# Kernel tuning notes

Hardware: AMD Instinct MI355X
Metric: run time of the kernel (lower is better)

Reference implementation:

```python
import jax, jax.numpy as jnp
import numpy as np


def setup_inputs() -> dict:
    key = jax.random.key(0)
    k1, k2, k3, k4, k5 = jax.random.split(key, 5)
    B, S, IN, OUT, R = 4, 2048, 4096, 4096, 16
    x = jax.random.normal(k1, (B, S, IN), dtype=jnp.float32)
    weight = jax.random.normal(k2, (OUT, IN), dtype=jnp.float32) * 0.02
    bias = jax.random.normal(k3, (OUT,), dtype=jnp.float32) * 0.02
    lora_A = jax.random.normal(k4, (R, IN), dtype=jnp.float32) * 0.02
    lora_B = jax.random.normal(k5, (OUT, R), dtype=jnp.float32) * 0.02
    return {"x": x, "weight": weight, "bias": bias, "lora_A": lora_A, "lora_B": lora_B}


def reference(x, weight, bias, lora_A, lora_B):
    # HiRA (Linear path): out = x @ (W * (1 + A^T B^T)^T)^T + bias
    # prod_AB[i, o] = sum_r A[r, i] * B[o, r]; adapted_weight[o, i] = W[o, i] * (prod_AB + 1)[i, o]
    prod_AB = jnp.einsum('ri,or->io', lora_A, lora_B) + 1.0       # [in, out]
    adapted_weight = weight * prod_AB.T                            # [out, in]
    # F.linear: x @ adapted_weight^T + bias
    return jnp.einsum('bsi,oi->bso', x, adapted_weight) + bias
```

## Files before the change

kernel.cpp:

```cpp
#include <hip/hip_runtime.h>
#include <hip/hip_bf16.h>
#include <stdint.h>

#define M_DIM 8192
#define N_DIM 4096
#define K_DIM 4096
#define R_DIM 16

typedef __bf16 bf16x8 __attribute__((ext_vector_type(8)));
typedef float f32x4 __attribute__((ext_vector_type(4)));
typedef unsigned short u16x8 __attribute__((ext_vector_type(8)));

#define AS1(p) ((const __attribute__((address_space(1))) void*)(p))
#define AS3(p) ((__attribute__((address_space(3))) void*)(p))

#define BAR() do { asm volatile("" ::: "memory"); __builtin_amdgcn_s_barrier(); asm volatile("" ::: "memory"); } while (0)
#define VMCNT2() asm volatile("s_waitcnt vmcnt(2)" ::: "memory")
#define VMCNT0() asm volatile("s_waitcnt vmcnt(0)" ::: "memory")
#define VMCNT8() asm volatile("s_waitcnt vmcnt(8)" ::: "memory")

__device__ __forceinline__ unsigned short f2bf(float f) {
  unsigned u = __builtin_bit_cast(unsigned, f);
  u += 0x7FFFu + ((u >> 16) & 1u);
  return (unsigned short)(u >> 16);
}

#define CVT_BLOCKS 4096
__global__ void __launch_bounds__(256) prep_kernel(
    const float* __restrict__ x, const float* __restrict__ W,
    const float* __restrict__ lA, const float* __restrict__ lB,
    unsigned short* __restrict__ xb, unsigned short* __restrict__ awb) {
  __shared__ float Asub[16 * 512];
  __shared__ float Bsub[32 * 16];
  const int tid = threadIdx.x;

  if (blockIdx.x < 1024) {
    const int i0 = (blockIdx.x & 7) * 512;
    const int o0 = (blockIdx.x >> 3) * 32;
    for (int idx = tid; idx < 16 * 512; idx += 256) {
      int r = idx >> 9, i = idx & 511;
      Asub[idx] = lA[r * K_DIM + i0 + i];
    }
    for (int idx = tid; idx < 32 * 16; idx += 256) {
      int o = idx >> 4, r = idx & 15;
      Bsub[idx] = lB[(o0 + o) * R_DIM + r];
    }
    __syncthreads();
    for (int idx = tid; idx < 32 * 512; idx += 256) {
      int o = idx >> 9, i = idx & 511;
      float s = 1.0f;
#pragma unroll
      for (int r = 0; r < 16; ++r) s += Asub[r * 512 + i] * Bsub[o * 16 + r];
      size_t g = (size_t)(o0 + o) * K_DIM + i0 + i;
      awb[g] = f2bf(W[g] * s);
    }
  } else {
    const long total = (long)M_DIM * K_DIM;
    long i = ((long)(blockIdx.x - 1024) * 256 + tid) * 8;
    const long stride = (long)CVT_BLOCKS * 256 * 8;
    for (; i < total; i += stride) {
      const float4* p = (const float4*)(x + i);
      float4 f0 = p[0], f1 = p[1];
      u16x8 v;
      v[0] = f2bf(f0.x); v[1] = f2bf(f0.y); v[2] = f2bf(f0.z); v[3] = f2bf(f0.w);
      v[4] = f2bf(f1.x); v[5] = f2bf(f1.y); v[6] = f2bf(f1.z); v[7] = f2bf(f1.w);
      *(u16x8*)(xb + i) = v;
    }
  }
}

__global__ void __launch_bounds__(512, 2) gemm_kernel(
    const unsigned short* __restrict__ Ag,
    const unsigned short* __restrict__ Bg,
    const float* __restrict__ bias,
    float* __restrict__ out) {
  __shared__ __attribute__((aligned(16))) unsigned short LDS[2 * 32768];

  const int nwg = gridDim.x;
  const int q8 = nwg >> 3;
  const int wg = blockIdx.x;
  const int swz = (wg & 7) * q8 + (wg >> 3);
  const int tiles_n = N_DIM / 256;
  const int brow = (swz / tiles_n) * 256;
  const int bcol = (swz % tiles_n) * 256;

  const int tid = threadIdx.x;
  const int lane = tid & 63;
  const int w = tid >> 6;
  const int wr = w >> 2, wc = w & 3;
  const int fr = lane & 15;
  const int kq = (lane >> 4) << 3;

  const int rr = lane >> 2;
  const int cc = ((lane & 1) << 3) | ((((lane >> 1) ^ (lane >> 5)) & 1) << 4);
  const int c_sw = ((w & 1) << 5) | cc;
  const int rbase = ((w >> 1) << 4) + rr;

  const unsigned short* srcA[2][2];
#pragma unroll
  for (int h = 0; h < 2; ++h)
#pragma unroll
    for (int q = 0; q < 2; ++q)
      srcA[h][q] = Ag + (size_t)(brow + h * 128 + q * 64 + rbase) * K_DIM + c_sw;
  const long long bdelta = (long long)(Bg - Ag) + (long long)(bcol - brow) * K_DIM;

  auto stageA = [&](int buf, int h, int kt) {
#pragma unroll
    for (int q = 0; q < 2; ++q)
      __builtin_amdgcn_global_load_lds(AS1(srcA[h][q] + (size_t)kt * 64),
          AS3(&LDS[buf * 32768 + h * 8192 + q * 4096 + w * 512]), 16, 0, 0);
  };
  auto stageB = [&](int buf, int h, int kt) {
#pragma unroll
    for (int q = 0; q < 2; ++q)
      __builtin_amdgcn_global_load_lds(AS1(srcA[h][q] + bdelta + (size_t)kt * 64),
          AS3(&LDS[buf * 32768 + 16384 + h * 8192 + q * 4096 + w * 512]), 16, 0, 0);
  };

  const int rdsw = ((fr << 6) | (kq << 1)) ^ ((fr & 8) << 2);
  auto lda = [&](int buf, int m, int kk) -> bf16x8 {
    return *(const bf16x8*)((const char*)LDS +
        (buf * 65536 + wr * 16384 + (m * 2 + kk) * 1024 + rdsw));
  };
  auto ldb = [&](int buf, int n, int kk) -> bf16x8 {
    return *(const bf16x8*)((const char*)LDS +
        (buf * 65536 + 32768 + (wc >> 1) * 16384 +
         (((wc & 1) * 4 + n) * 2 + kk) * 1024 + rdsw));
  };

  f32x4 acc[8][4] = {};
  bf16x8 a[2][4];
  bf16x8 blo[2][2], bhi[2][2];

  auto read_a = [&](int buf, int mg) {
#pragma unroll
    for (int kk = 0; kk < 2; ++kk)
#pragma unroll
      for (int mi = 0; mi < 4; ++mi)
        a[kk][mi] = lda(buf, mg + mi, kk);
  };
  auto read_blo = [&](int buf) {
#pragma unroll
    for (int kk = 0; kk < 2; ++kk)
#pragma unroll
      for (int ni = 0; ni < 2; ++ni)
        blo[kk][ni] = ldb(buf, ni, kk);
  };
  auto read_bhi = [&](int buf) {
#pragma unroll
    for (int kk = 0; kk < 2; ++kk)
#pragma unroll
      for (int ni = 0; ni < 2; ++ni)
        bhi[kk][ni] = ldb(buf, 2 + ni, kk);
  };
  auto mma_b = [&](bf16x8 (&bb)[2][2], int am, int an) {
#pragma unroll
    for (int mi = 0; mi < 4; ++mi)
#pragma unroll
      for (int ni = 0; ni < 2; ++ni)
#pragma unroll
        for (int kk = 0; kk < 2; ++kk)
          acc[am + mi][an + ni] = __builtin_amdgcn_mfma_f32_16x16x32_bf16(
              a[kk][mi], bb[kk][ni], acc[am + mi][an + ni], 0, 0, 0);
  };

  auto tile_body = [&](int t, int buf, bool g2, bool gr) {
    const int nxbuf = buf ^ 1;
    __builtin_amdgcn_s_setprio(1); mma_b(blo, 0, 0); __builtin_amdgcn_s_setprio(0);
    BAR();
    if (g2) stageB(buf, 0, t + 2);
    __builtin_amdgcn_s_setprio(1); mma_b(bhi, 0, 2); __builtin_amdgcn_s_setprio(0);
    read_a(buf, 4);
    if (g2) { VMCNT2(); } else { VMCNT0(); }
    BAR();
    if (g2) { stageB(buf, 1, t + 2); stageA(buf, 0, t + 2); }
    __builtin_amdgcn_s_setprio(1); mma_b(bhi, 4, 2); __builtin_amdgcn_s_setprio(0);
    if (gr) read_bhi(nxbuf);
    BAR();
    if (g2) stageA(buf, 1, t + 2);
    __builtin_amdgcn_s_setprio(1); mma_b(blo, 4, 0); __builtin_amdgcn_s_setprio(0);
    if (gr) { read_a(nxbuf, 0); read_blo(nxbuf); }
    BAR();
  };

  stageB(0, 0, 0); stageB(0, 1, 0); stageA(0, 0, 0); stageA(0, 1, 0);
  stageB(1, 0, 1); stageB(1, 1, 1); stageA(1, 0, 1); stageA(1, 1, 1);
  VMCNT8();
  BAR();
  read_bhi(0); read_a(0, 0); read_blo(0);

#pragma unroll 1
  for (int i = 0; i < 32; ++i) {
    const bool more = (i < 31);
    tile_body(2 * i,     0, more, true);
    tile_body(2 * i + 1, 1, more, more);
  }

  const int fq = (lane >> 4) * 4;
#pragma unroll
  for (int n = 0; n < 4; ++n) {
    const int col = bcol + wc * 64 + n * 16 + fr;
    const float bb = bias[col];
#pragma unroll
    for (int m = 0; m < 8; ++m) {
      const int row = brow + wr * 128 + m * 16 + fq;
      f32x4 v = acc[m][n];
#pragma unroll
      for (int j = 0; j < 4; ++j)
        out[(size_t)(row + j) * N_DIM + col] = v[j] + bb;
    }
  }
}

extern "C" void kernel_launch(void* const* d_in, const int* in_sizes, int n_in,
                              void* d_out, int out_size, void* d_ws, size_t ws_size,
                              hipStream_t stream) {
  const float* x    = (const float*)d_in[0];
  const float* W    = (const float*)d_in[1];
  const float* bias = (const float*)d_in[2];
  const float* lA   = (const float*)d_in[3];
  const float* lB   = (const float*)d_in[4];
  float* out = (float*)d_out;

  unsigned short* xb  = (unsigned short*)d_ws;
  unsigned short* awb = xb + (size_t)M_DIM * K_DIM;

  prep_kernel<<<1024 + CVT_BLOCKS, 256, 0, stream>>>(x, W, lA, lB, xb, awb);
  gemm_kernel<<<(M_DIM / 256) * (N_DIM / 256), 512, 0, stream>>>(xb, awb, bias, out);
}
```

Baseline: 294.1 us.

## Load GEMM B operand directly from global into registers, bypassing LDS

The weight (B) tile is no longer staged through LDS. Each wave now loads its B fragments directly from global memory into registers one K-tile ahead, which halves LDS usage and removes one barrier per tile. The tile order is also changed to walk rows first within each column of output tiles, and the vmcnt waits are retuned to the new load counts. In exchange, B is fetched redundantly by the two wave rows, depends on the L2 cache for reuse, and a full vmcnt(0) drain is now taken mid-tile, which can expose global load latency.

Measured after the change: 473.7 us. 61.0% more time.

```diff
diff --git a/kernel.cpp b/kernel.cpp
--- a/kernel.cpp
+++ b/kernel.cpp
@@ -15,9 +15,9 @@
 #define AS3(p) ((__attribute__((address_space(3))) void*)(p))
 
 #define BAR() do { asm volatile("" ::: "memory"); __builtin_amdgcn_s_barrier(); asm volatile("" ::: "memory"); } while (0)
-#define VMCNT2() asm volatile("s_waitcnt vmcnt(2)" ::: "memory")
-#define VMCNT0() asm volatile("s_waitcnt vmcnt(0)" ::: "memory")
-#define VMCNT8() asm volatile("s_waitcnt vmcnt(8)" ::: "memory")
+#define VMCNT4()  asm volatile("s_waitcnt vmcnt(4)" ::: "memory")
+#define VMCNT0()  asm volatile("s_waitcnt vmcnt(0)" ::: "memory")
+#define VMCNT12() asm volatile("s_waitcnt vmcnt(12)" ::: "memory")
 
 __device__ __forceinline__ unsigned short f2bf(float f) {
   unsigned u = __builtin_bit_cast(unsigned, f);
@@ -74,15 +74,14 @@
     const unsigned short* __restrict__ Bg,
     const float* __restrict__ bias,
     float* __restrict__ out) {
-  __shared__ __attribute__((aligned(16))) unsigned short LDS[2 * 32768];
+  __shared__ __attribute__((aligned(16))) unsigned short LDS[2 * 16384];
 
   const int nwg = gridDim.x;
   const int q8 = nwg >> 3;
   const int wg = blockIdx.x;
   const int swz = (wg & 7) * q8 + (wg >> 3);
-  const int tiles_n = N_DIM / 256;
-  const int brow = (swz / tiles_n) * 256;
-  const int bcol = (swz % tiles_n) * 256;
+  const int brow = (swz & 31) * 256;
+  const int bcol = (swz >> 5) * 256;
 
   const int tid = threadIdx.x;
   const int lane = tid & 63;
@@ -102,31 +101,24 @@
 #pragma unroll
     for (int q = 0; q < 2; ++q)
       srcA[h][q] = Ag + (size_t)(brow + h * 128 + q * 64 + rbase) * K_DIM + c_sw;
-  const long long bdelta = (long long)(Bg - Ag) + (long long)(bcol - brow) * K_DIM;
 
   auto stageA = [&](int buf, int h, int kt) {
 #pragma unroll
     for (int q = 0; q < 2; ++q)
       __builtin_amdgcn_global_load_lds(AS1(srcA[h][q] + (size_t)kt * 64),
-          AS3(&LDS[buf * 32768 + h * 8192 + q * 4096 + w * 512]), 16, 0, 0);
-  };
-  auto stageB = [&](int buf, int h, int kt) {
-#pragma unroll
-    for (int q = 0; q < 2; ++q)
-      __builtin_amdgcn_global_load_lds(AS1(srcA[h][q] + bdelta + (size_t)kt * 64),
-          AS3(&LDS[buf * 32768 + 16384 + h * 8192 + q * 4096 + w * 512]), 16, 0, 0);
+          AS3(&LDS[buf * 16384 + h * 8192 + q * 4096 + w * 512]), 16, 0, 0);
   };
 
   const int rdsw = ((fr << 6) | (kq << 1)) ^ ((fr & 8) << 2);
   auto lda = [&](int buf, int m, int kk) -> bf16x8 {
     return *(const bf16x8*)((const char*)LDS +
-        (buf * 65536 + wr * 16384 + (m * 2 + kk) * 1024 + rdsw));
-  };
-  auto ldb = [&](int buf, int n, int kk) -> bf16x8 {
-    return *(const bf16x8*)((const char*)LDS +
-        (buf * 65536 + 32768 + (wc >> 1) * 16384 +
-         (((wc & 1) * 4 + n) * 2 + kk) * 1024 + rdsw));
-  };
+        (buf * 32768 + wr * 16384 + (m * 2 + kk) * 1024 + rdsw));
+  };
+
+  const unsigned short* bp[4];
+#pragma unroll
+  for (int n = 0; n < 4; ++n)
+    bp[n] = Bg + (size_t)(bcol + wc * 64 + n * 16 + fr) * K_DIM + kq;
 
   f32x4 acc[8][4] = {};
   bf16x8 a[2][4];
@@ -139,19 +131,19 @@
       for (int mi = 0; mi < 4; ++mi)
         a[kk][mi] = lda(buf, mg + mi, kk);
   };
-  auto read_blo = [&](int buf) {
+  auto load_blo = [&](int t) {
 #pragma unroll
     for (int kk = 0; kk < 2; ++kk)
 #pragma unroll
       for (int ni = 0; ni < 2; ++ni)
-        blo[kk][ni] = ldb(buf, ni, kk);
-  };
-  auto read_bhi = [&](int buf) {
+        blo[kk][ni] = *(const bf16x8*)(bp[ni] + (size_t)t * 64 + kk * 32);
+  };
+  auto load_bhi = [&](int t) {
 #pragma unroll
     for (int kk = 0; kk < 2; ++kk)
 #pragma unroll
       for (int ni = 0; ni < 2; ++ni)
-        bhi[kk][ni] = ldb(buf, 2 + ni, kk);
+        bhi[kk][ni] = *(const bf16x8*)(bp[2 + ni] + (size_t)t * 64 + kk * 32);
   };
   auto mma_b = [&](bf16x8 (&bb)[2][2], int am, int an) {
 #pragma unroll
@@ -166,28 +158,27 @@
 
   auto tile_body = [&](int t, int buf, bool g2, bool gr) {
     const int nxbuf = buf ^ 1;
+    VMCNT4();
     __builtin_amdgcn_s_setprio(1); mma_b(blo, 0, 0); __builtin_amdgcn_s_setprio(0);
-    BAR();
-    if (g2) stageB(buf, 0, t + 2);
+    VMCNT0();
     __builtin_amdgcn_s_setprio(1); mma_b(bhi, 0, 2); __builtin_amdgcn_s_setprio(0);
     read_a(buf, 4);
-    if (g2) { VMCNT2(); } else { VMCNT0(); }
     BAR();
-    if (g2) { stageB(buf, 1, t + 2); stageA(buf, 0, t + 2); }
+    if (g2) stageA(buf, 0, t + 2), stageA(buf, 1, t + 2);
+    __builtin_amdgcn_s_setprio(1); mma_b(blo, 4, 0); __builtin_amdgcn_s_setprio(0);
+    if (gr) load_blo(t + 1);
     __builtin_amdgcn_s_setprio(1); mma_b(bhi, 4, 2); __builtin_amdgcn_s_setprio(0);
-    if (gr) read_bhi(nxbuf);
+    if (gr) load_bhi(t + 1);
+    if (gr) read_a(nxbuf, 0);
     BAR();
-    if (g2) stageA(buf, 1, t + 2);
-    __builtin_amdgcn_s_setprio(1); mma_b(blo, 4, 0); __builtin_amdgcn_s_setprio(0);
-    if (gr) { read_a(nxbuf, 0); read_blo(nxbuf); }
-    BAR();
-  };
-
-  stageB(0, 0, 0); stageB(0, 1, 0); stageA(0, 0, 0); stageA(0, 1, 0);
-  stageB(1, 0, 1); stageB(1, 1, 1); stageA(1, 0, 1); stageA(1, 1, 1);
-  VMCNT8();
+  };
+
+  stageA(0, 0, 0); stageA(0, 1, 0);
+  stageA(1, 0, 1); stageA(1, 1, 1);
+  load_blo(0); load_bhi(0);
+  VMCNT12();
   BAR();
-  read_bhi(0); read_a(0, 0); read_blo(0);
+  read_a(0, 0);
 
 #pragma unroll 1
   for (int i = 0; i < 32; ++i) {
```
